# Kernel tuning notes

Hardware: AMD Instinct MI355X
Metric: run time of the kernel (lower is better)

Reference implementation:

```python
import jax, jax.numpy as jnp
import numpy as np

N = 8192
IN_F = 512
OUT_F = 64
ALPHA = 0.2   # LeakyReLU negative slope
STDV = 0.2
NEG_INF = -9e15


def setup_inputs() -> dict:
    key = jax.random.key(0)
    k1, k2, k3, k4 = jax.random.split(key, 4)
    x = jax.random.normal(k1, (N, IN_F), dtype=jnp.float32)
    adj = jax.random.randint(k2, (N, N), 0, 2, dtype=jnp.int32)
    W = jax.random.normal(k3, (IN_F, OUT_F), dtype=jnp.float32) * STDV
    a = jax.random.normal(k4, (2 * OUT_F, 1), dtype=jnp.float32) * STDV
    return {"x": x, "adj": adj, "W": W, "a": a}


def reference(x, adj, W, a):
    # Wh: [N, F']
    Wh = x @ W
    # attention logits: e[i,j] = leakyrelu(Wh[i]@a1 + Wh[j]@a2)
    Wh1 = Wh @ a[:OUT_F, :]   # [N, 1]
    Wh2 = Wh @ a[OUT_F:, :]   # [N, 1]
    e = Wh1 + Wh2.T           # [N, N] via broadcast
    e = jnp.where(e >= 0, e, ALPHA * e)  # LeakyReLU
    # mask by adjacency, row softmax
    masked = jnp.where(adj > 0, e, jnp.float32(NEG_INF))
    attention = jax.nn.softmax(masked, axis=1)
    # dropout rate is 0.0 in this config -> identity
    h_prime = attention @ Wh  # [N, F']
    out = jnp.where(h_prime > 0, h_prime, jnp.expm1(h_prime))  # ELU
    return out, attention
```

## Files before the change

kernel.cpp:

```cpp
#include <hip/hip_runtime.h>
#include <cmath>

#define Nn    8192
#define INF_  512
#define OUTF  64

typedef __attribute__((ext_vector_type(4))) int   i4;
typedef __attribute__((ext_vector_type(4))) float f4v;
typedef __attribute__((ext_vector_type(8))) short s8;
typedef __attribute__((ext_vector_type(4))) float f32x4;
typedef unsigned long long u64;

__device__ __forceinline__ float lrelu(float v) { return fmaxf(v, 0.2f * v); }

__device__ __forceinline__ unsigned int f2bf(float f) {
    unsigned int u = __float_as_uint(f);
    u = (u + 0x7FFFu + ((u >> 16) & 1u)) >> 16;
    return u;
}

__global__ __launch_bounds__(1024, 8) void k1_wh(
    const float* __restrict__ x, const float* __restrict__ W,
    const float* __restrict__ a, unsigned short* __restrict__ WhT,
    float* __restrict__ Wh1, float* __restrict__ Wh2)
{
    __shared__ float xs[16][520];
    __shared__ float part[3][16][64];
    __shared__ unsigned short stage[64][16];
    const int t    = threadIdx.x;
    const int row0 = blockIdx.x * 16;

    #pragma unroll
    for (int s2 = 0; s2 < 2; ++s2) {
        const int idx = s2 * 4096 + 4 * t;
        const f4v v = __builtin_nontemporal_load(
            (const f4v*)(x + (size_t)row0 * INF_ + idx));
        *(f4v*)&xs[idx >> 9][idx & 511] = v;
    }
    __syncthreads();

    const int s    = t >> 8;
    const int r    = (t >> 4) & 15;
    const int cg   = (t & 15) << 2;
    const int row  = row0 + r;
    const float* __restrict__ Wp = W + (size_t)s * 128 * OUTF;

    float4 acc = make_float4(0.f, 0.f, 0.f, 0.f);
    for (int k = 0; k < 128; k += 4) {
        const float4 xv = *(const float4*)&xs[r][s * 128 + k];
        const float* wp = Wp + (size_t)k * OUTF + cg;
        const float4 w0 = *(const float4*)(wp);
        const float4 w1 = *(const float4*)(wp + OUTF);
        const float4 w2 = *(const float4*)(wp + 2 * OUTF);
        const float4 w3 = *(const float4*)(wp + 3 * OUTF);
        acc.x += xv.x * w0.x + xv.y * w1.x + xv.z * w2.x + xv.w * w3.x;
        acc.y += xv.x * w0.y + xv.y * w1.y + xv.z * w2.y + xv.w * w3.y;
        acc.z += xv.x * w0.z + xv.y * w1.z + xv.z * w2.z + xv.w * w3.z;
        acc.w += xv.x * w0.w + xv.y * w1.w + xv.z * w2.w + xv.w * w3.w;
    }
    if (s > 0) *(float4*)&part[s - 1][r][cg] = acc;
    __syncthreads();
    if (s == 0) {
        const float4 pa = *(const float4*)&part[0][r][cg];
        const float4 pb = *(const float4*)&part[1][r][cg];
        const float4 pc = *(const float4*)&part[2][r][cg];
        acc.x += pa.x + pb.x + pc.x;
        acc.y += pa.y + pb.y + pc.y;
        acc.z += pa.z + pb.z + pc.z;
        acc.w += pa.w + pb.w + pc.w;
        stage[cg + 0][r] = (unsigned short)f2bf(acc.x);
        stage[cg + 1][r] = (unsigned short)f2bf(acc.y);
        stage[cg + 2][r] = (unsigned short)f2bf(acc.z);
        stage[cg + 3][r] = (unsigned short)f2bf(acc.w);

        float p1 = acc.x * a[cg]        + acc.y * a[cg + 1]
                 + acc.z * a[cg + 2]    + acc.w * a[cg + 3];
        float p2 = acc.x * a[OUTF + cg]     + acc.y * a[OUTF + cg + 1]
                 + acc.z * a[OUTF + cg + 2] + acc.w * a[OUTF + cg + 3];
        #pragma unroll
        for (int off = 8; off; off >>= 1) {
            p1 += __shfl_xor(p1, off);
            p2 += __shfl_xor(p2, off);
        }
        if ((t & 15) == 0) { Wh1[row] = p1; Wh2[row] = p2; }
    }
    __syncthreads();
    if (t < 256) {
        const int col = t >> 2;
        const int q   = t & 3;
        const u64 v = *(const u64*)&stage[col][q * 4];
        *(u64*)(WhT + (size_t)col * Nn + row0 + q * 4) = v;
    }
}

__global__ __launch_bounds__(1024, 8) void k2_fused(
    const int* __restrict__ adj, const unsigned short* __restrict__ WhT,
    const float* __restrict__ Wh1, const float* __restrict__ Wh2,
    float* __restrict__ outp, float* __restrict__ att)
{
    __shared__ unsigned char bm8[16][2048];
    __shared__ alignas(16) unsigned short att_t[2][16 * 256];
    __shared__ float red[3][4][16][16];
    __shared__ float sm_Sp[16][16];
    __shared__ float sm_is[16];

    const int t    = threadIdx.x;
    const int lane = t & 63;
    const int w    = t >> 6;
    const int row0 = blockIdx.x * 16;

    const int j0 = 4 * t;
    const f4v w4a = *(const f4v*)(Wh2 + j0);
    const f4v w4b = *(const f4v*)(Wh2 + 4096 + j0);

    {
        const i4* __restrict__ asrc = (const i4*)(adj + (size_t)row0 * Nn);
        float Sp = 0.f;
        i4 p0 = __builtin_nontemporal_load(asrc + t);
        i4 p1 = __builtin_nontemporal_load(asrc + 1024 + t);
        i4 p2 = __builtin_nontemporal_load(asrc + 2048 + t);
        #pragma unroll
        for (int s = 0; s < 32; ++s) {
            const int r = s >> 1, h = s & 1;
            const i4 av = p0;
            p0 = p1; p1 = p2;
            if (s < 29)
                p2 = __builtin_nontemporal_load(asrc + (s + 3) * 1024 + t);
            const f4v w4 = h ? w4b : w4a;
            const float h1r = Wh1[row0 + r];
            const int nib = (av.x != 0 ? 1 : 0) | (av.y != 0 ? 2 : 0)
                          | (av.z != 0 ? 4 : 0) | (av.w != 0 ? 8 : 0);
            Sp += (nib & 1) ? __expf(lrelu(h1r + w4.x)) : 0.f;
            Sp += (nib & 2) ? __expf(lrelu(h1r + w4.y)) : 0.f;
            Sp += (nib & 4) ? __expf(lrelu(h1r + w4.z)) : 0.f;
            Sp += (nib & 8) ? __expf(lrelu(h1r + w4.w)) : 0.f;
            bm8[r][h * 1024 + t] = (unsigned char)nib;
            if (h) {
                #pragma unroll
                for (int off = 32; off; off >>= 1) Sp += __shfl_xor(Sp, off);
                if (lane == 0) sm_Sp[r][w] = Sp;
                Sp = 0.f;
            }
        }
    }
    __syncthreads();

    {
        float sv = sm_Sp[w][lane & 15];
        #pragma unroll
        for (int off = 8; off; off >>= 1) sv += __shfl_xor(sv, off);
        if (lane == 0) sm_is[w] = 1.0f / sv;
    }
    __syncthreads();

    const int row = row0 + w;
    const float h1 = Wh1[row];
    const float is = sm_is[w];

    const int ct = w & 3;
    const int kq = w >> 2;
    f32x4 acc = {0.f, 0.f, 0.f, 0.f};

    auto produce = [&](int c, int bf) {
        const int jb = c * 256;
        const f4v w2 = *((const f4v*)(Wh2 + jb) + lane);
        const int nib = bm8[w][c * 64 + lane];
        const float v0 = (nib & 1) ? __expf(lrelu(h1 + w2.x)) * is : 0.f;
        const float v1 = (nib & 2) ? __expf(lrelu(h1 + w2.y)) * is : 0.f;
        const float v2 = (nib & 4) ? __expf(lrelu(h1 + w2.z)) * is : 0.f;
        const float v3 = (nib & 8) ? __expf(lrelu(h1 + w2.w)) * is : 0.f;
        f4v st; st.x = v0; st.y = v1; st.z = v2; st.w = v3;
        __builtin_nontemporal_store(st, (f4v*)(att + (size_t)row * Nn + jb) + lane);
        const u64 pk = (u64)(f2bf(v0) | (f2bf(v1) << 16))
                     | ((u64)(f2bf(v2) | (f2bf(v3) << 16)) << 32);
        int byte = w * 512 + lane * 8;  byte ^= (w & 7) << 4;
        *(u64*)((char*)att_t[bf] + byte) = pk;
    };

    const int ar = lane & 15;
    const int ag = lane >> 4;
    auto bload = [&](int c, int ss) -> s8 {
        const int ks = kq * 2 + ss;
        return *(const s8*)(WhT + (size_t)(ct * 16 + ar) * Nn
                            + c * 256 + ks * 32 + ag * 8);
    };
    auto amfma = [&](int bf, s8 b0, s8 b1) {
        #pragma unroll
        for (int ss = 0; ss < 2; ++ss) {
            const int ks = kq * 2 + ss;
            int byte = ar * 512 + ks * 64 + ag * 16;
            byte ^= (ar & 7) << 4;
            const s8 af = *(const s8*)((char*)att_t[bf] + byte);
            acc = __builtin_amdgcn_mfma_f32_16x16x32_bf16(af, ss ? b1 : b0, acc, 0, 0, 0);
        }
    };

    s8 b0 = bload(0, 0), b1 = bload(0, 1);
    produce(0, 0);
    asm volatile("s_waitcnt lgkmcnt(0)" ::: "memory");
    __builtin_amdgcn_s_barrier();
    for (int c = 0; c < Nn / 256 - 1; ++c) {
        produce(c + 1, (c + 1) & 1);
        const s8 nb0 = bload(c + 1, 0);
        const s8 nb1 = bload(c + 1, 1);
        amfma(c & 1, b0, b1);
        asm volatile("s_waitcnt lgkmcnt(0)" ::: "memory");
        __builtin_amdgcn_s_barrier();
        b0 = nb0; b1 = nb1;
    }
    amfma((Nn / 256 - 1) & 1, b0, b1);

    __syncthreads();
    if (kq > 0) {
        #pragma unroll
        for (int q = 0; q < 4; ++q) red[kq - 1][ct][ag * 4 + q][ar] = acc[q];
    }
    __syncthreads();
    if (kq == 0) {
        #pragma unroll
        for (int q = 0; q < 4; ++q) {
            const int r = ag * 4 + q;
            float v = acc[q] + red[0][ct][r][ar] + red[1][ct][r][ar] + red[2][ct][r][ar];
            v = v > 0.f ? v : expm1f(v);
            outp[(size_t)(row0 + r) * OUTF + ct * 16 + ar] = v;
        }
    }
}

extern "C" void kernel_launch(void* const* d_in, const int* in_sizes, int n_in,
                              void* d_out, int out_size, void* d_ws, size_t ws_size,
                              hipStream_t stream)
{
    const float* x   = (const float*)d_in[0];
    const int*   adj = (const int*)d_in[1];
    const float* W   = (const float*)d_in[2];
    const float* a   = (const float*)d_in[3];

    float* outp = (float*)d_out;
    float* att  = outp + (size_t)Nn * OUTF;

    float* Wh1 = (float*)d_ws;
    float* Wh2 = Wh1 + Nn;
    unsigned short* WhT = (unsigned short*)(Wh2 + Nn);

    hipLaunchKernelGGL(k1_wh,    dim3(Nn / 16), dim3(1024), 0, stream,
                       x, W, a, WhT, Wh1, Wh2);
    hipLaunchKernelGGL(k2_fused, dim3(Nn / 16), dim3(1024), 0, stream,
                       adj, WhT, Wh1, Wh2, outp, att);
}
```

Before: 160.2 us.

## Write attention rows during the adjacency pass with per-row barrier normalization

The fp32 attention store moves out of the MFMA produce loop and into the first adjacency-scan pass. After each row's partial sums are reduced, a block barrier lets every thread read the row's softmax denominator, scale its held exp values and store them immediately. The aim is to overlap the large attention write with the adjacency read stream and to lighten the main loop. The cost is sixteen block-wide barriers in the scan phase instead of one, plus extra registers for the held values.

Result: slower. 192.1 us (+19.9%).

```diff
diff --git a/kernel.cpp b/kernel.cpp
--- a/kernel.cpp
+++ b/kernel.cpp
@@ -115,7 +115,9 @@
 
     {
         const i4* __restrict__ asrc = (const i4*)(adj + (size_t)row0 * Nn);
+        float* __restrict__ attb = att + (size_t)row0 * Nn;
         float Sp = 0.f;
+        float pq0 = 0.f, pq1 = 0.f, pq2 = 0.f, pq3 = 0.f;
         i4 p0 = __builtin_nontemporal_load(asrc + t);
         i4 p1 = __builtin_nontemporal_load(asrc + 1024 + t);
         i4 p2 = __builtin_nontemporal_load(asrc + 2048 + t);
@@ -130,26 +132,34 @@
             const float h1r = Wh1[row0 + r];
             const int nib = (av.x != 0 ? 1 : 0) | (av.y != 0 ? 2 : 0)
                           | (av.z != 0 ? 4 : 0) | (av.w != 0 ? 8 : 0);
-            Sp += (nib & 1) ? __expf(lrelu(h1r + w4.x)) : 0.f;
-            Sp += (nib & 2) ? __expf(lrelu(h1r + w4.y)) : 0.f;
-            Sp += (nib & 4) ? __expf(lrelu(h1r + w4.z)) : 0.f;
-            Sp += (nib & 8) ? __expf(lrelu(h1r + w4.w)) : 0.f;
+            const float q0 = (nib & 1) ? __expf(lrelu(h1r + w4.x)) : 0.f;
+            const float q1 = (nib & 2) ? __expf(lrelu(h1r + w4.y)) : 0.f;
+            const float q2 = (nib & 4) ? __expf(lrelu(h1r + w4.z)) : 0.f;
+            const float q3 = (nib & 8) ? __expf(lrelu(h1r + w4.w)) : 0.f;
+            Sp += (q0 + q1) + (q2 + q3);
             bm8[r][h * 1024 + t] = (unsigned char)nib;
-            if (h) {
+            if (!h) {
+                pq0 = q0; pq1 = q1; pq2 = q2; pq3 = q3;
+            } else {
                 #pragma unroll
                 for (int off = 32; off; off >>= 1) Sp += __shfl_xor(Sp, off);
                 if (lane == 0) sm_Sp[r][w] = Sp;
                 Sp = 0.f;
+                asm volatile("s_waitcnt lgkmcnt(0)" ::: "memory");
+                __builtin_amdgcn_s_barrier();
+                float sv = 0.f;
+                #pragma unroll
+                for (int kk = 0; kk < 16; ++kk) sv += sm_Sp[r][kk];
+                const float isr = 1.0f / sv;
+                if (t == 0) sm_is[r] = isr;
+                f4v sa; sa.x = pq0 * isr; sa.y = pq1 * isr;
+                        sa.z = pq2 * isr; sa.w = pq3 * isr;
+                f4v sb; sb.x = q0 * isr;  sb.y = q1 * isr;
+                        sb.z = q2 * isr;  sb.w = q3 * isr;
+                __builtin_nontemporal_store(sa, (f4v*)(attb + (size_t)r * Nn + j0));
+                __builtin_nontemporal_store(sb, (f4v*)(attb + (size_t)r * Nn + 4096 + j0));
             }
         }
-    }
-    __syncthreads();
-
-    {
-        float sv = sm_Sp[w][lane & 15];
-        #pragma unroll
-        for (int off = 8; off; off >>= 1) sv += __shfl_xor(sv, off);
-        if (lane == 0) sm_is[w] = 1.0f / sv;
     }
     __syncthreads();
 
@@ -169,8 +179,6 @@
         const float v1 = (nib & 2) ? __expf(lrelu(h1 + w2.y)) * is : 0.f;
         const float v2 = (nib & 4) ? __expf(lrelu(h1 + w2.z)) * is : 0.f;
         const float v3 = (nib & 8) ? __expf(lrelu(h1 + w2.w)) * is : 0.f;
-        f4v st; st.x = v0; st.y = v1; st.z = v2; st.w = v3;
-        __builtin_nontemporal_store(st, (f4v*)(att + (size_t)row * Nn + jb) + lane);
         const u64 pk = (u64)(f2bf(v0) | (f2bf(v1) << 16))
                      | ((u64)(f2bf(v2) | (f2bf(v3) << 16)) << 32);
         int byte = w * 512 + lane * 8;  byte ^= (w & 7) << 4;
```

## Split fused attention kernel into adjacency scan and bitmask-driven PV kernels

Applied to the files above, without the earlier changes.

Splits the fused kernel into two. The first reads adj, computes the softmax denominators and writes a packed 1-bit-per-entry adjacency mask to global memory. The second uses 512 threads per block with a 128-column chunk loop, recomputes the attention values from the bitmask, writes att and runs the bf16 MFMA product against WhT. The intent is to decouple the adj-bandwidth phase from the att-write/MFMA phase and cut shared memory use so more blocks fit per CU. In exchange it adds a kernel launch, a global round trip for the mask and denominators, and drops the explicit register prefetch of B fragments.

Result: slower. 176.1 us (+9.9%).

```diff
diff --git a/kernel.cpp b/kernel.cpp
--- a/kernel.cpp
+++ b/kernel.cpp
@@ -6,6 +6,7 @@
 #define OUTF  64
 
 typedef __attribute__((ext_vector_type(4))) int   i4;
+typedef __attribute__((ext_vector_type(2))) float f2;
 typedef __attribute__((ext_vector_type(4))) float f4v;
 typedef __attribute__((ext_vector_type(8))) short s8;
 typedef __attribute__((ext_vector_type(4))) float f32x4;
@@ -17,6 +18,14 @@
     unsigned int u = __float_as_uint(f);
     u = (u + 0x7FFFu + ((u >> 16) & 1u)) >> 16;
     return u;
+}
+
+__device__ __forceinline__ u64 pack32(u64 v) {
+    v &= 0x0F0F0F0F0F0F0F0FULL;
+    v = (v | (v >> 4))  & 0x00FF00FF00FF00FFULL;
+    v = (v | (v >> 8))  & 0x0000FFFF0000FFFFULL;
+    v = (v | (v >> 16)) & 0x00000000FFFFFFFFULL;
+    return v;
 }
 
 __global__ __launch_bounds__(1024, 8) void k1_wh(
@@ -93,16 +102,13 @@
     }
 }
 
-__global__ __launch_bounds__(1024, 8) void k2_fused(
-    const int* __restrict__ adj, const unsigned short* __restrict__ WhT,
-    const float* __restrict__ Wh1, const float* __restrict__ Wh2,
-    float* __restrict__ outp, float* __restrict__ att)
+__global__ __launch_bounds__(1024, 8) void k2a_scan(
+    const int* __restrict__ adj, const float* __restrict__ Wh1,
+    const float* __restrict__ Wh2, u64* __restrict__ bm_g,
+    float* __restrict__ is_g)
 {
     __shared__ unsigned char bm8[16][2048];
-    __shared__ alignas(16) unsigned short att_t[2][16 * 256];
-    __shared__ float red[3][4][16][16];
     __shared__ float sm_Sp[16][16];
-    __shared__ float sm_is[16];
 
     const int t    = threadIdx.x;
     const int lane = t & 63;
@@ -149,80 +155,110 @@
         float sv = sm_Sp[w][lane & 15];
         #pragma unroll
         for (int off = 8; off; off >>= 1) sv += __shfl_xor(sv, off);
-        if (lane == 0) sm_is[w] = 1.0f / sv;
-    }
-    __syncthreads();
-
-    const int row = row0 + w;
-    const float h1 = Wh1[row];
-    const float is = sm_is[w];
+        if (lane == 0) is_g[row0 + w] = 1.0f / sv;
+    }
+
+    #pragma unroll
+    for (int i = 0; i < 2; ++i) {
+        const int wi = 2 * t + i;
+        const int r  = wi >> 7, c = wi & 127;
+        const u64 v0 = *(const u64*)&bm8[r][16 * c];
+        const u64 v1 = *(const u64*)&bm8[r][16 * c + 8];
+        bm_g[(size_t)(row0 + r) * 128 + c] = pack32(v0) | (pack32(v1) << 32);
+    }
+}
+
+__global__ __launch_bounds__(512) void k2b_pv(
+    const unsigned short* __restrict__ WhT, const float* __restrict__ Wh1,
+    const float* __restrict__ Wh2, const u64* __restrict__ bm_g,
+    const float* __restrict__ is_g,
+    float* __restrict__ outp, float* __restrict__ att)
+{
+    __shared__ alignas(16) unsigned short att_t[2][16 * 128];
+    __shared__ float red[4][16][16];
+
+    const int t    = threadIdx.x;
+    const int lane = t & 63;
+    const int w    = t >> 6;
+    const int row0 = blockIdx.x * 16;
+
+    const int rA = 2 * w, rB = 2 * w + 1;
+    const float h1A = Wh1[row0 + rA], isA = is_g[row0 + rA];
+    const float h1B = Wh1[row0 + rB], isB = is_g[row0 + rB];
+    const u64* __restrict__ bmA = bm_g + (size_t)(row0 + rA) * (Nn / 64);
+    const u64* __restrict__ bmB = bm_g + (size_t)(row0 + rB) * (Nn / 64);
 
     const int ct = w & 3;
-    const int kq = w >> 2;
+    const int kh = w >> 2;
     f32x4 acc = {0.f, 0.f, 0.f, 0.f};
 
-    auto produce = [&](int c, int bf) {
-        const int jb = c * 256;
-        const f4v w2 = *((const f4v*)(Wh2 + jb) + lane);
-        const int nib = bm8[w][c * 64 + lane];
-        const float v0 = (nib & 1) ? __expf(lrelu(h1 + w2.x)) * is : 0.f;
-        const float v1 = (nib & 2) ? __expf(lrelu(h1 + w2.y)) * is : 0.f;
-        const float v2 = (nib & 4) ? __expf(lrelu(h1 + w2.z)) * is : 0.f;
-        const float v3 = (nib & 8) ? __expf(lrelu(h1 + w2.w)) * is : 0.f;
-        f4v st; st.x = v0; st.y = v1; st.z = v2; st.w = v3;
-        __builtin_nontemporal_store(st, (f4v*)(att + (size_t)row * Nn + jb) + lane);
-        const u64 pk = (u64)(f2bf(v0) | (f2bf(v1) << 16))
-                     | ((u64)(f2bf(v2) | (f2bf(v3) << 16)) << 32);
-        int byte = w * 512 + lane * 8;  byte ^= (w & 7) << 4;
-        *(u64*)((char*)att_t[bf] + byte) = pk;
+    const int j2   = lane * 2;
+    const int wsub = j2 >> 6;
+    const int bit0 = j2 & 63;
+
+    auto produce = [&](int c, int b) {
+        const int jb = c * 128;
+        const f2 w2 = *((const f2*)(Wh2 + jb) + lane);
+        const int wi = (jb >> 6) + wsub;
+        {
+            const u64 bA = bmA[wi];
+            const float v0 = ((bA >> bit0) & 1ull)       ? __expf(lrelu(h1A + w2.x)) * isA : 0.f;
+            const float v1 = ((bA >> (bit0 + 1)) & 1ull) ? __expf(lrelu(h1A + w2.y)) * isA : 0.f;
+            f2 st; st.x = v0; st.y = v1;
+            __builtin_nontemporal_store(st, (f2*)(att + (size_t)(row0 + rA) * Nn + jb) + lane);
+            const unsigned int pk = f2bf(v0) | (f2bf(v1) << 16);
+            int byte = rA * 256 + j2 * 2;  byte ^= (rA & 7) << 4;
+            *(unsigned int*)((char*)att_t[b] + byte) = pk;
+        }
+        {
+            const u64 bB = bmB[wi];
+            const float v0 = ((bB >> bit0) & 1ull)       ? __expf(lrelu(h1B + w2.x)) * isB : 0.f;
+            const float v1 = ((bB >> (bit0 + 1)) & 1ull) ? __expf(lrelu(h1B + w2.y)) * isB : 0.f;
+            f2 st; st.x = v0; st.y = v1;
+            __builtin_nontemporal_store(st, (f2*)(att + (size_t)(row0 + rB) * Nn + jb) + lane);
+            const unsigned int pk = f2bf(v0) | (f2bf(v1) << 16);
+            int byte = rB * 256 + j2 * 2;  byte ^= (rB & 7) << 4;
+            *(unsigned int*)((char*)att_t[b] + byte) = pk;
+        }
     };
 
-    const int ar = lane & 15;
-    const int ag = lane >> 4;
-    auto bload = [&](int c, int ss) -> s8 {
-        const int ks = kq * 2 + ss;
-        return *(const s8*)(WhT + (size_t)(ct * 16 + ar) * Nn
-                            + c * 256 + ks * 32 + ag * 8);
+    const int arow = lane & 15;
+    const int agrp = lane >> 4;
+    auto domfma = [&](int c, int b) {
+        const int jb = c * 128;
+        #pragma unroll
+        for (int s = 0; s < 2; ++s) {
+            const int ks = kh * 2 + s;
+            int byte = arow * 256 + ks * 64 + agrp * 16;
+            byte ^= (arow & 7) << 4;
+            const s8 afrag = *(const s8*)((char*)att_t[b] + byte);
+            const s8 bfrag = *(const s8*)(WhT + (size_t)(ct * 16 + arow) * Nn
+                                          + jb + ks * 32 + agrp * 8);
+            acc = __builtin_amdgcn_mfma_f32_16x16x32_bf16(afrag, bfrag, acc, 0, 0, 0);
+        }
     };
-    auto amfma = [&](int bf, s8 b0, s8 b1) {
-        #pragma unroll
-        for (int ss = 0; ss < 2; ++ss) {
-            const int ks = kq * 2 + ss;
-            int byte = ar * 512 + ks * 64 + ag * 16;
-            byte ^= (ar & 7) << 4;
-            const s8 af = *(const s8*)((char*)att_t[bf] + byte);
-            acc = __builtin_amdgcn_mfma_f32_16x16x32_bf16(af, ss ? b1 : b0, acc, 0, 0, 0);
-        }
-    };
-
-    s8 b0 = bload(0, 0), b1 = bload(0, 1);
+
     produce(0, 0);
-    asm volatile("s_waitcnt lgkmcnt(0)" ::: "memory");
-    __builtin_amdgcn_s_barrier();
-    for (int c = 0; c < Nn / 256 - 1; ++c) {
+    __syncthreads();
+    for (int c = 0; c < Nn / 128 - 1; ++c) {
         produce(c + 1, (c + 1) & 1);
-        const s8 nb0 = bload(c + 1, 0);
-        const s8 nb1 = bload(c + 1, 1);
-        amfma(c & 1, b0, b1);
-        asm volatile("s_waitcnt lgkmcnt(0)" ::: "memory");
-        __builtin_amdgcn_s_barrier();
-        b0 = nb0; b1 = nb1;
-    }
-    amfma((Nn / 256 - 1) & 1, b0, b1);
-
-    __syncthreads();
-    if (kq > 0) {
-        #pragma unroll
-        for (int q = 0; q < 4; ++q) red[kq - 1][ct][ag * 4 + q][ar] = acc[q];
-    }
-    __syncthreads();
-    if (kq == 0) {
+        domfma(c, c & 1);
+        __syncthreads();
+    }
+    domfma(Nn / 128 - 1, (Nn / 128 - 1) & 1);
+
+    __syncthreads();
+    if (kh == 1) {
+        #pragma unroll
+        for (int q = 0; q < 4; ++q) red[ct][agrp * 4 + q][arow] = acc[q];
+    }
+    __syncthreads();
+    if (kh == 0) {
         #pragma unroll
         for (int q = 0; q < 4; ++q) {
-            const int r = ag * 4 + q;
-            float v = acc[q] + red[0][ct][r][ar] + red[1][ct][r][ar] + red[2][ct][r][ar];
+            float v = acc[q] + red[ct][agrp * 4 + q][arow];
             v = v > 0.f ? v : expm1f(v);
-            outp[(size_t)(row0 + r) * OUTF + ct * 16 + ar] = v;
+            outp[(size_t)(row0 + agrp * 4 + q) * OUTF + ct * 16 + arow] = v;
         }
     }
 }
@@ -239,12 +275,16 @@
     float* outp = (float*)d_out;
     float* att  = outp + (size_t)Nn * OUTF;
 
-    float* Wh1 = (float*)d_ws;
-    float* Wh2 = Wh1 + Nn;
-    unsigned short* WhT = (unsigned short*)(Wh2 + Nn);
+    float* Wh1  = (float*)d_ws;
+    float* Wh2  = Wh1 + Nn;
+    float* is_g = Wh2 + Nn;
+    unsigned short* WhT = (unsigned short*)(is_g + Nn);
+    u64* bm_g = (u64*)(WhT + (size_t)OUTF * Nn);
 
     hipLaunchKernelGGL(k1_wh,    dim3(Nn / 16), dim3(1024), 0, stream,
                        x, W, a, WhT, Wh1, Wh2);
-    hipLaunchKernelGGL(k2_fused, dim3(Nn / 16), dim3(1024), 0, stream,
-                       adj, WhT, Wh1, Wh2, outp, att);
-}
+    hipLaunchKernelGGL(k2a_scan, dim3(Nn / 16), dim3(1024), 0, stream,
+                       adj, Wh1, Wh2, bm_g, is_g);
+    hipLaunchKernelGGL(k2b_pv,   dim3(Nn / 16), dim3(512), 0, stream,
+                       WhT, Wh1, Wh2, bm_g, is_g, outp, att);
+}
```
